# Kernel tuning notes

Hardware: AMD Instinct MI355X
Metric: run time of the kernel (lower is better)

## Reference

```python
import jax, jax.numpy as jnp
import numpy as np

# Multi-scale feature pyramid (H, W) per level
LEVEL_SHAPES = ((48, 160), (24, 80), (12, 40), (6, 20))
LEN = sum(h * w for h, w in LEVEL_SHAPES)  # 10200 flattened tokens
B, D, NH, NL, NP, DFF, NLAYERS = 2, 256, 8, 4, 4, 1024, 3
DH = D // NH
# offset normalizer is (W, H) per level, matching Deformable-DETR
NORMALIZER = np.array([[w, h] for h, w in LEVEL_SHAPES], dtype=np.float32)
LEVEL_START = np.cumsum([0] + [h * w for h, w in LEVEL_SHAPES])[:-1]


def layer_norm(x, g, b, eps=1e-5):
    m = jnp.mean(x, -1, keepdims=True)
    v = jnp.var(x, -1, keepdims=True)
    return (x - m) * jax.lax.rsqrt(v + eps) * g + b


def get_reference_points(valid_ratios):
    # valid_ratios: [B, NL, 2] (ratio_w, ratio_h)
    refs = []
    for lvl, (Hl, Wl) in enumerate(LEVEL_SHAPES):
        ry, rx = jnp.meshgrid(jnp.linspace(0.5, Hl - 0.5, Hl, dtype=jnp.float32),
                              jnp.linspace(0.5, Wl - 0.5, Wl, dtype=jnp.float32), indexing='ij')
        ry = ry.reshape(-1)[None] / (valid_ratios[:, None, lvl, 1] * Hl)
        rx = rx.reshape(-1)[None] / (valid_ratios[:, None, lvl, 0] * Wl)
        refs.append(jnp.stack([rx, ry], -1))
    ref = jnp.concatenate(refs, 1)                      # [B, LEN, 2]
    return ref[:, :, None] * valid_ratios[:, None]      # [B, LEN, NL, 2]


def bilinear_sample(value_bh, loc, Hl, Wl):
    # value_bh: [B, NH, Hl*Wl, DH]; loc: [B, Lq, NH, NP, 2] in [0,1]
    # grid_sample semantics: bilinear, zero padding, align_corners=False
    x = loc[..., 0] * Wl - 0.5
    y = loc[..., 1] * Hl - 0.5
    x0f = jnp.floor(x); y0f = jnp.floor(y)
    fx = x - x0f; fy = y - y0f
    x0 = x0f.astype(jnp.int32); y0 = y0f.astype(jnp.int32)
    Lq = loc.shape[1]
    out = jnp.zeros((B, NH, Lq * NP, DH), loc.dtype)
    for dy in (0, 1):
        for dx in (0, 1):
            xi = x0 + dx; yi = y0 + dy
            w = (fx if dx else 1.0 - fx) * (fy if dy else 1.0 - fy)
            valid = (xi >= 0) & (xi < Wl) & (yi >= 0) & (yi < Hl)
            idx = jnp.clip(yi, 0, Hl - 1) * Wl + jnp.clip(xi, 0, Wl - 1)  # [B,Lq,NH,NP]
            idx = jnp.transpose(idx, (0, 2, 1, 3)).reshape(B, NH, Lq * NP)
            v = jnp.take_along_axis(value_bh, idx[..., None], axis=2)    # [B,NH,Lq*NP,DH]
            wm = jnp.transpose(jnp.where(valid, w, 0.0), (0, 2, 1, 3)).reshape(B, NH, Lq * NP)
            out = out + v * wm[..., None]
    return out


def ms_deform_attn(q, src, ref, Woff, boff, Wattn, battn, Wval, bval, Wout, bout):
    Lq = q.shape[1]
    off = (q @ Woff + boff).reshape(B, Lq, NH, NL, NP, 2)
    attn = jax.nn.softmax((q @ Wattn + battn).reshape(B, Lq, NH, NL * NP), -1)
    attn = attn.reshape(B, Lq, NH, NL, NP)
    val = (src @ Wval + bval).reshape(B, LEN, NH, DH).transpose(0, 2, 1, 3)  # [B,NH,LEN,DH]
    norm = jnp.asarray(NORMALIZER)
    loc = ref[:, :, None, :, None, :] + off / norm[None, None, None, :, None, :]
    out = jnp.zeros((B, NH, Lq, DH), q.dtype)
    for lvl, (Hl, Wl) in enumerate(LEVEL_SHAPES):
        s = int(LEVEL_START[lvl])
        vl = val[:, :, s:s + Hl * Wl]
        sampled = bilinear_sample(vl, loc[:, :, :, lvl], Hl, Wl).reshape(B, NH, Lq, NP, DH)
        out = out + jnp.einsum('bhqpd,bqhp->bhqd', sampled, attn[:, :, :, lvl])
    out = out.transpose(0, 2, 1, 3).reshape(B, Lq, D)
    return out @ Wout + bout


def reference(src, pos, valid_ratios, W_off, b_off, W_attn, b_attn, W_val, b_val,
              W_out, b_out, ln1_g, ln1_b, W_ff1, b_ff1, W_ff2, b_ff2, ln2_g, ln2_b):
    ref = get_reference_points(valid_ratios)
    x = src
    for l in range(NLAYERS):
        q = x + pos
        att = ms_deform_attn(q, x, ref, W_off[l], b_off[l], W_attn[l], b_attn[l],
                             W_val[l], b_val[l], W_out[l], b_out[l])
        x = layer_norm(x + att, ln1_g[l], ln1_b[l])
        h = jax.nn.relu(x @ W_ff1[l] + b_ff1[l]) @ W_ff2[l] + b_ff2[l]
        x = layer_norm(x + h, ln2_g[l], ln2_b[l])
    return x


def setup_inputs() -> dict:
    key = jax.random.key(0)
    ks = jax.random.split(key, 12)
    s = 0.02
    return {
        'src': jax.random.normal(ks[0], (B, LEN, D), jnp.float32),
        'pos': jax.random.normal(ks[1], (B, LEN, D), jnp.float32),
        'valid_ratios': jnp.ones((B, NL, 2), jnp.float32),
        'W_off': jax.random.normal(ks[2], (NLAYERS, D, NH * NL * NP * 2), jnp.float32) * s,
        'b_off': jax.random.normal(ks[3], (NLAYERS, NH * NL * NP * 2), jnp.float32) * s,
        'W_attn': jax.random.normal(ks[4], (NLAYERS, D, NH * NL * NP), jnp.float32) * s,
        'b_attn': jax.random.normal(ks[5], (NLAYERS, NH * NL * NP), jnp.float32) * s,
        'W_val': jax.random.normal(ks[6], (NLAYERS, D, D), jnp.float32) * s,
        'b_val': jnp.zeros((NLAYERS, D), jnp.float32),
        'W_out': jax.random.normal(ks[7], (NLAYERS, D, D), jnp.float32) * s,
        'b_out': jnp.zeros((NLAYERS, D), jnp.float32),
        'ln1_g': jnp.ones((NLAYERS, D), jnp.float32),
        'ln1_b': jnp.zeros((NLAYERS, D), jnp.float32),
        'W_ff1': jax.random.normal(ks[8], (NLAYERS, D, DFF), jnp.float32) * s,
        'b_ff1': jnp.zeros((NLAYERS, DFF), jnp.float32),
        'W_ff2': jax.random.normal(ks[9], (NLAYERS, DFF, D), jnp.float32) * s,
        'b_ff2': jnp.zeros((NLAYERS, D), jnp.float32),
        'ln2_g': jnp.ones((NLAYERS, D), jnp.float32),
        'ln2_b': jnp.zeros((NLAYERS, D), jnp.float32),
    }
```

## Files before the change

kernel.cpp:

```cpp
#include <hip/hip_runtime.h>

typedef short bf16x8 __attribute__((ext_vector_type(8)));
typedef float f32x4  __attribute__((ext_vector_type(4)));

#define LEN_TOT 10200
#define BB 2
#define DD 256
#define NHH 8
#define NLL 4
#define NPP 4
#define DHH 32
#define DFF_ 1024
#define ROWS (BB * LEN_TOT)

__device__ inline unsigned short f2bf(float f) {
    unsigned int u = __float_as_uint(f);
    u += 0x7fffu + ((u >> 16) & 1u);
    return (unsigned short)(u >> 16);
}
__device__ inline unsigned int pack2(float a, float b) {
    return (unsigned int)f2bf(a) | ((unsigned int)f2bf(b) << 16);
}

__global__ __launch_bounds__(256) void ref_points_kernel(
    const float* __restrict__ vr, float* __restrict__ ref)
{
    int i = blockIdx.x * blockDim.x + threadIdx.x;
    if (i >= BB * LEN_TOT) return;
    int b = i / LEN_TOT, pos = i % LEN_TOT;
    int lvl, st, Hl, Wl;
    if (pos < 7680)      { lvl = 0; st = 0;     Hl = 48; Wl = 160; }
    else if (pos < 9600) { lvl = 1; st = 7680;  Hl = 24; Wl = 80;  }
    else if (pos < 10080){ lvl = 2; st = 9600;  Hl = 12; Wl = 40;  }
    else                 { lvl = 3; st = 10080; Hl = 6;  Wl = 20;  }
    int local = pos - st;
    int row = local / Wl, col = local % Wl;
    float rx = (col + 0.5f) / (vr[(b * NLL + lvl) * 2 + 0] * (float)Wl);
    float ry = (row + 0.5f) / (vr[(b * NLL + lvl) * 2 + 1] * (float)Hl);
    #pragma unroll
    for (int ol = 0; ol < NLL; ++ol) {
        ref[((size_t)i * NLL + ol) * 2 + 0] = rx * vr[(b * NLL + ol) * 2 + 0];
        ref[((size_t)i * NLL + ol) * 2 + 1] = ry * vr[(b * NLL + ol) * 2 + 1];
    }
}

__global__ __launch_bounds__(256) void convert_src_kernel(
    const float* __restrict__ src, float* __restrict__ x,
    unsigned short* __restrict__ xb, int n8)
{
    int i = blockIdx.x * blockDim.x + threadIdx.x;
    if (i >= n8) return;
    float4 a = ((const float4*)src)[2 * i];
    float4 b = ((const float4*)src)[2 * i + 1];
    ((float4*)x)[2 * i]     = a;
    ((float4*)x)[2 * i + 1] = b;
    uint4 o;
    o.x = pack2(a.x, a.y); o.y = pack2(a.z, a.w);
    o.z = pack2(b.x, b.y); o.w = pack2(b.z, b.w);
    ((uint4*)xb)[i] = o;
}

__global__ __launch_bounds__(256) void addq_kernel(
    const float* __restrict__ x, const float* __restrict__ p,
    unsigned short* __restrict__ qb, int n8)
{
    int i = blockIdx.x * blockDim.x + threadIdx.x;
    if (i >= n8) return;
    float4 a0 = ((const float4*)x)[2 * i];
    float4 a1 = ((const float4*)x)[2 * i + 1];
    float4 b0 = ((const float4*)p)[2 * i];
    float4 b1 = ((const float4*)p)[2 * i + 1];
    uint4 o;
    o.x = pack2(a0.x + b0.x, a0.y + b0.y);
    o.y = pack2(a0.z + b0.z, a0.w + b0.w);
    o.z = pack2(a1.x + b1.x, a1.y + b1.y);
    o.w = pack2(a1.z + b1.z, a1.w + b1.w);
    ((uint4*)qb)[i] = o;
}

__global__ __launch_bounds__(256) void wt_kernel(
    const float* __restrict__ W, unsigned short* __restrict__ WT,
    int K, int N, int ldOut, int rowOff)
{
    __shared__ float t[32][33];
    const float* Wl = W + (size_t)blockIdx.z * K * N;
    unsigned short* WTl = WT + (size_t)blockIdx.z * ldOut;
    int kb = blockIdx.x * 32, nb = blockIdx.y * 32;
    int tx = threadIdx.x, ty = threadIdx.y;
    #pragma unroll
    for (int i = 0; i < 4; ++i)
        t[ty + i * 8][tx] = Wl[(size_t)(kb + ty + i * 8) * N + nb + tx];
    __syncthreads();
    #pragma unroll
    for (int i = 0; i < 4; ++i)
        WTl[(size_t)(rowOff + nb + ty + i * 8) * K + kb + tx] = f2bf(t[tx][ty + i * 8]);
}

__global__ __launch_bounds__(256) void bias_oa_kernel(
    const float* __restrict__ b_off, const float* __restrict__ b_attn,
    float* __restrict__ out)
{
    int i = blockIdx.x * blockDim.x + threadIdx.x;
    if (i >= 3 * 384) return;
    int l = i / 384, j = i % 384;
    out[i] = (j < 256) ? b_off[l * 256 + j] : b_attn[l * 128 + (j - 256)];
}

template<int OUTMODE>
__global__ __launch_bounds__(256) void gemm_bf16(
    const unsigned short* __restrict__ A,
    const unsigned short* __restrict__ BT,
    const float* __restrict__ bias,
    void* __restrict__ Cout,
    int M, int N, int K)
{
    __shared__ short lds[2 * 128 * 64];
    const int tid = threadIdx.x;
    const int l   = tid & 63;
    const int wid = tid >> 6;
    const int wm  = wid >> 1, wn = wid & 1;
    const int lrow = l & 15, lkg = l >> 4;
    const int rowBase = blockIdx.x * 128;
    const int colBase = blockIdx.y * 128;

    const int srow  = tid >> 3;
    const int sslot = tid & 7;

    f32x4 acc[4][4] = {};

    for (int k0 = 0; k0 < K; k0 += 64) {
        #pragma unroll
        for (int rr = 0; rr < 128; rr += 32) {
            int r = rr + srow;
            int sw = (sslot ^ (r & 7)) * 8;
            int gr = rowBase + r; if (gr > M - 1) gr = M - 1;
            uint4 av = *(const uint4*)(A + (size_t)gr * K + k0 + sslot * 8);
            *(uint4*)&lds[r * 64 + sw] = av;
            int n = colBase + r;
            uint4 bv = *(const uint4*)(BT + (size_t)n * K + k0 + sslot * 8);
            *(uint4*)&lds[8192 + r * 64 + sw] = bv;
        }
        __syncthreads();
        #pragma unroll
        for (int kk = 0; kk < 2; ++kk) {
            int kslot = kk * 4 + lkg;
            int ssw = (kslot ^ (lrow & 7)) * 8;
            bf16x8 af[4], bfr[4];
            #pragma unroll
            for (int mi = 0; mi < 4; ++mi)
                af[mi] = *(const bf16x8*)&lds[(wm * 64 + mi * 16 + lrow) * 64 + ssw];
            #pragma unroll
            for (int ni = 0; ni < 4; ++ni)
                bfr[ni] = *(const bf16x8*)&lds[8192 + (wn * 64 + ni * 16 + lrow) * 64 + ssw];
            #pragma unroll
            for (int mi = 0; mi < 4; ++mi)
                #pragma unroll
                for (int ni = 0; ni < 4; ++ni)
                    acc[mi][ni] = __builtin_amdgcn_mfma_f32_16x16x32_bf16(
                        af[mi], bfr[ni], acc[mi][ni], 0, 0, 0);
        }
        __syncthreads();
    }

    #pragma unroll
    for (int ni = 0; ni < 4; ++ni) {
        int col = colBase + wn * 64 + ni * 16 + lrow;
        float bv = bias[col];
        #pragma unroll
        for (int mi = 0; mi < 4; ++mi) {
            int r0 = rowBase + wm * 64 + mi * 16 + lkg * 4;
            #pragma unroll
            for (int j = 0; j < 4; ++j) {
                int r = r0 + j;
                if (r < M) {
                    float v = acc[mi][ni][j] + bv;
                    if (OUTMODE == 0) {
                        ((float*)Cout)[(size_t)r * N + col] = v;
                    } else {
                        if (OUTMODE == 1) v = fmaxf(v, 0.f);
                        ((unsigned short*)Cout)[(size_t)r * N + col] = f2bf(v);
                    }
                }
            }
        }
    }
}

__global__ __launch_bounds__(256) void sample_kernel(
    const unsigned short* __restrict__ valb,
    const float* __restrict__ oa,
    const float* __restrict__ ref,
    unsigned short* __restrict__ out)
{
    __shared__ int2 ent[8][64];

    const int tid = threadIdx.x;
    const int il = tid >> 5;
    const int L  = tid & 31;
    const int item = blockIdx.x * 8 + il;
    const int h  = item & (NHH - 1);
    const int bq = item >> 3;
    const int b  = bq / LEN_TOT;

    const float* row = oa + (size_t)bq * 384;

    {
        int p = L >> 1, dy = L & 1;
        int lvl = p >> 2;
        int Wl = 160 >> lvl, Hl = 48 >> lvl;
        int ST = (lvl == 0) ? 0 : ((lvl == 1) ? 7680 : ((lvl == 2) ? 9600 : 10080));

        float logit = row[256 + h * 16 + p];
        float m = logit;
        #pragma unroll
        for (int mk = 1; mk <= 16; mk <<= 1) m = fmaxf(m, __shfl_xor(m, mk));
        float e = __expf(logit - m);
        float s = e;
        #pragma unroll
        for (int mk = 1; mk <= 16; mk <<= 1) s += __shfl_xor(s, mk);
        float a = 2.f * e / s;

        float rx = ref[bq * 8 + lvl * 2 + 0];
        float ry = ref[bq * 8 + lvl * 2 + 1];
        float ox = row[h * 32 + p * 2 + 0];
        float oy = row[h * 32 + p * 2 + 1];
        float xx = fmaf(rx, (float)Wl, ox) - 0.5f;
        float yy = fmaf(ry, (float)Hl, oy) - 0.5f;
        float xf = floorf(xx), yf = floorf(yy);
        float fx = xx - xf, fy = yy - yf;
        int x0 = (int)xf, y0 = (int)yf;
        int yi = y0 + dy;
        float wy = dy ? fy : 1.f - fy;
        bool vy = (yi >= 0) && (yi < Hl);
        int yc = min(max(yi, 0), Hl - 1);
        int base = (b * LEN_TOT + ST) * 256 + h * 32;
        #pragma unroll
        for (int dx = 0; dx < 2; ++dx) {
            int xi = x0 + dx;
            float wx = dx ? fx : 1.f - fx;
            bool valid = vy && (xi >= 0) && (xi < Wl);
            int xc = min(max(xi, 0), Wl - 1);
            float w = valid ? a * wx * wy : 0.f;
            ent[il][p * 4 + dy * 2 + dx] =
                make_int2(base + (yc * Wl + xc) * 256, __float_as_int(w));
        }
    }
    __syncthreads();

    float acc = 0.f;
    #pragma unroll 16
    for (int e2 = 0; e2 < 64; ++e2) {
        int2 d = ent[il][e2];
        unsigned short uv = valb[(size_t)d.x + L];
        float v = __uint_as_float((unsigned int)uv << 16);
        acc = fmaf(__int_as_float(d.y), v, acc);
    }
    out[(size_t)item * DHH + L] = f2bf(acc);
}

__global__ __launch_bounds__(256) void resln_kernel(
    float* __restrict__ x, const float* __restrict__ r,
    const float* __restrict__ g, const float* __restrict__ bta,
    unsigned short* __restrict__ xb)
{
    int row = blockIdx.x * 4 + (threadIdx.x >> 6);
    int lane = threadIdx.x & 63;
    if (row >= ROWS) return;
    float4 v  = *(const float4*)(x + (size_t)row * DD + lane * 4);
    float4 rr = *(const float4*)(r + (size_t)row * DD + lane * 4);
    v.x += rr.x; v.y += rr.y; v.z += rr.z; v.w += rr.w;
    float s  = v.x + v.y + v.z + v.w;
    float s2 = v.x * v.x + v.y * v.y + v.z * v.z + v.w * v.w;
    #pragma unroll
    for (int o = 1; o < 64; o <<= 1) {
        s  += __shfl_xor(s, o);
        s2 += __shfl_xor(s2, o);
    }
    float mean = s * (1.f / DD);
    float var  = s2 * (1.f / DD) - mean * mean;
    float inv  = rsqrtf(var + 1e-5f);
    float4 gg = *(const float4*)(g + lane * 4);
    float4 bb = *(const float4*)(bta + lane * 4);
    float4 o;
    o.x = (v.x - mean) * inv * gg.x + bb.x;
    o.y = (v.y - mean) * inv * gg.y + bb.y;
    o.z = (v.z - mean) * inv * gg.z + bb.z;
    o.w = (v.w - mean) * inv * gg.w + bb.w;
    *(float4*)(x + (size_t)row * DD + lane * 4) = o;
    uint2 ob;
    ob.x = pack2(o.x, o.y);
    ob.y = pack2(o.z, o.w);
    ((uint2*)(xb + (size_t)row * DD))[lane] = ob;
}

extern "C" void kernel_launch(void* const* d_in, const int* in_sizes, int n_in,
                              void* d_out, int out_size, void* d_ws, size_t ws_size,
                              hipStream_t stream)
{
    const float* src    = (const float*)d_in[0];
    const float* pos    = (const float*)d_in[1];
    const float* vr     = (const float*)d_in[2];
    const float* W_off  = (const float*)d_in[3];
    const float* b_off  = (const float*)d_in[4];
    const float* W_attn = (const float*)d_in[5];
    const float* b_attn = (const float*)d_in[6];
    const float* W_val  = (const float*)d_in[7];
    const float* b_val  = (const float*)d_in[8];
    const float* W_out  = (const float*)d_in[9];
    const float* b_out  = (const float*)d_in[10];
    const float* ln1_g  = (const float*)d_in[11];
    const float* ln1_b  = (const float*)d_in[12];
    const float* W_ff1  = (const float*)d_in[13];
    const float* b_ff1  = (const float*)d_in[14];
    const float* W_ff2  = (const float*)d_in[15];
    const float* b_ff2  = (const float*)d_in[16];
    const float* ln2_g  = (const float*)d_in[17];
    const float* ln2_b  = (const float*)d_in[18];

    float* x = (float*)d_out;
    float* ws = (float*)d_ws;
    size_t o = 0;
    float* oa      = ws + o; o += (size_t)ROWS * 384;
    float* tmp     = ws + o; o += (size_t)ROWS * 256;
    float* ref     = ws + o; o += (size_t)ROWS * 8;
    float* bias_oa = ws + o; o += 3 * 384;

    unsigned short* ub = (unsigned short*)(ws + o);
    size_t uo = 0;
    unsigned short* q_bf    = ub + uo; uo += (size_t)ROWS * 256;
    unsigned short* x_bf    = ub + uo; uo += (size_t)ROWS * 256;
    unsigned short* samp_bf = ub + uo; uo += (size_t)ROWS * 256;
    unsigned short* val_bf  = ub + uo; uo += (size_t)ROWS * 256;
    unsigned short* h_bf    = ub + uo; uo += (size_t)ROWS * DFF_;
    unsigned short* WT_oa   = ub + uo; uo += (size_t)3 * 384 * 256;
    unsigned short* WT_val  = ub + uo; uo += (size_t)3 * 256 * 256;
    unsigned short* WT_out  = ub + uo; uo += (size_t)3 * 256 * 256;
    unsigned short* WT_ff1  = ub + uo; uo += (size_t)3 * 256 * 1024;
    unsigned short* WT_ff2  = ub + uo; uo += (size_t)3 * 1024 * 256;

    const int n8 = ROWS * DD / 8;

    convert_src_kernel<<<(n8 + 255) / 256, 256, 0, stream>>>(src, x, x_bf, n8);
    ref_points_kernel<<<(ROWS + 255) / 256, 256, 0, stream>>>(vr, ref);

    dim3 wtb(32, 8);
    wt_kernel<<<dim3(8,  8, 3), wtb, 0, stream>>>(W_off,  WT_oa,  256, 256,  384 * 256, 0);
    wt_kernel<<<dim3(8,  4, 3), wtb, 0, stream>>>(W_attn, WT_oa,  256, 128,  384 * 256, 256);
    wt_kernel<<<dim3(8,  8, 3), wtb, 0, stream>>>(W_val,  WT_val, 256, 256,  256 * 256, 0);
    wt_kernel<<<dim3(8,  8, 3), wtb, 0, stream>>>(W_out,  WT_out, 256, 256,  256 * 256, 0);
    wt_kernel<<<dim3(8, 32, 3), wtb, 0, stream>>>(W_ff1,  WT_ff1, 256, 1024, 256 * 1024, 0);
    wt_kernel<<<dim3(32, 8, 3), wtb, 0, stream>>>(W_ff2,  WT_ff2, 1024, 256, 1024 * 256, 0);
    bias_oa_kernel<<<(3 * 384 + 255) / 256, 256, 0, stream>>>(b_off, b_attn, bias_oa);

    dim3 g384(160, 3), g256(160, 2), g1024(160, 8);

    for (int l = 0; l < 3; ++l) {
        addq_kernel<<<(n8 + 255) / 256, 256, 0, stream>>>(x, pos, q_bf, n8);
        gemm_bf16<0><<<g384, 256, 0, stream>>>(
            q_bf, WT_oa + (size_t)l * 384 * 256, bias_oa + (size_t)l * 384, oa,
            ROWS, 384, 256);
        gemm_bf16<2><<<g256, 256, 0, stream>>>(
            x_bf, WT_val + (size_t)l * 65536, b_val + (size_t)l * 256, val_bf,
            ROWS, 256, 256);
        sample_kernel<<<ROWS * NHH / 8, 256, 0, stream>>>(
            val_bf, oa, ref, samp_bf);
        gemm_bf16<0><<<g256, 256, 0, stream>>>(
            samp_bf, WT_out + (size_t)l * 65536, b_out + (size_t)l * 256, tmp,
            ROWS, 256, 256);
        resln_kernel<<<(ROWS + 3) / 4, 256, 0, stream>>>(
            x, tmp, ln1_g + (size_t)l * 256, ln1_b + (size_t)l * 256, x_bf);
        gemm_bf16<1><<<g1024, 256, 0, stream>>>(
            x_bf, WT_ff1 + (size_t)l * 262144, b_ff1 + (size_t)l * 1024, h_bf,
            ROWS, 1024, 256);
        gemm_bf16<0><<<g256, 256, 0, stream>>>(
            h_bf, WT_ff2 + (size_t)l * 262144, b_ff2 + (size_t)l * 256, tmp,
            ROWS, 256, 1024);
        resln_kernel<<<(ROWS + 3) / 4, 256, 0, stream>>>(
            x, tmp, ln2_g + (size_t)l * 256, ln2_b + (size_t)l * 256, x_bf);
    }
}
```

Baseline: 730.8 us.

## Fuse query add into LN, bf16 offsets, direct-to-LDS GEMM loads, vectorized sampling

The per-layer addq kernel is removed: the first q is built in the conversion kernel and later ones in the second residual-LayerNorm kernel. The offset/attention GEMM now writes bf16 instead of fp32, which halves that buffer's traffic but makes sampling offsets and logits less precise. GEMM tile loads use global_load_lds so data goes straight into LDS without passing through registers. The sampling gather now reads 8 bf16 values per lane with 16-byte loads and reduces across lanes with shuffles, replacing scalar 2-byte gathers.

```diff
diff --git a/kernel.cpp b/kernel.cpp
--- a/kernel.cpp
+++ b/kernel.cpp
@@ -21,6 +21,9 @@
 __device__ inline unsigned int pack2(float a, float b) {
     return (unsigned int)f2bf(a) | ((unsigned int)f2bf(b) << 16);
 }
+__device__ inline float bflo(unsigned int u) { return __uint_as_float(u << 16); }
+__device__ inline float bfhi(unsigned int u) { return __uint_as_float(u & 0xffff0000u); }
+__device__ inline float bfs(unsigned short u) { return __uint_as_float((unsigned int)u << 16); }
 
 __global__ __launch_bounds__(256) void ref_points_kernel(
     const float* __restrict__ vr, float* __restrict__ ref)
@@ -45,8 +48,9 @@
 }
 
 __global__ __launch_bounds__(256) void convert_src_kernel(
-    const float* __restrict__ src, float* __restrict__ x,
-    unsigned short* __restrict__ xb, int n8)
+    const float* __restrict__ src, const float* __restrict__ pos,
+    float* __restrict__ x, unsigned short* __restrict__ xb,
+    unsigned short* __restrict__ qb, int n8)
 {
     int i = blockIdx.x * blockDim.x + threadIdx.x;
     if (i >= n8) return;
@@ -58,24 +62,14 @@
     o.x = pack2(a.x, a.y); o.y = pack2(a.z, a.w);
     o.z = pack2(b.x, b.y); o.w = pack2(b.z, b.w);
     ((uint4*)xb)[i] = o;
-}
-
-__global__ __launch_bounds__(256) void addq_kernel(
-    const float* __restrict__ x, const float* __restrict__ p,
-    unsigned short* __restrict__ qb, int n8)
-{
-    int i = blockIdx.x * blockDim.x + threadIdx.x;
-    if (i >= n8) return;
-    float4 a0 = ((const float4*)x)[2 * i];
-    float4 a1 = ((const float4*)x)[2 * i + 1];
-    float4 b0 = ((const float4*)p)[2 * i];
-    float4 b1 = ((const float4*)p)[2 * i + 1];
-    uint4 o;
-    o.x = pack2(a0.x + b0.x, a0.y + b0.y);
-    o.y = pack2(a0.z + b0.z, a0.w + b0.w);
-    o.z = pack2(a1.x + b1.x, a1.y + b1.y);
-    o.w = pack2(a1.z + b1.z, a1.w + b1.w);
-    ((uint4*)qb)[i] = o;
+    float4 p0 = ((const float4*)pos)[2 * i];
+    float4 p1 = ((const float4*)pos)[2 * i + 1];
+    uint4 oq;
+    oq.x = pack2(a.x + p0.x, a.y + p0.y);
+    oq.y = pack2(a.z + p0.z, a.w + p0.w);
+    oq.z = pack2(b.x + p1.x, b.y + p1.y);
+    oq.w = pack2(b.z + p1.z, b.w + p1.w);
+    ((uint4*)qb)[i] = oq;
 }
 
 __global__ __launch_bounds__(256) void wt_kernel(
@@ -123,22 +117,25 @@
     const int rowBase = blockIdx.x * 128;
     const int colBase = blockIdx.y * 128;
 
-    const int srow  = tid >> 3;
-    const int sslot = tid & 7;
-
     f32x4 acc[4][4] = {};
 
     for (int k0 = 0; k0 < K; k0 += 64) {
         #pragma unroll
-        for (int rr = 0; rr < 128; rr += 32) {
-            int r = rr + srow;
-            int sw = (sslot ^ (r & 7)) * 8;
+        for (int it = 0; it < 4; ++it) {
+            int sidx = tid + 256 * it;
+            int r = sidx >> 3;
+            int ss = ((sidx & 7) ^ (r & 7)) * 8;
             int gr = rowBase + r; if (gr > M - 1) gr = M - 1;
-            uint4 av = *(const uint4*)(A + (size_t)gr * K + k0 + sslot * 8);
-            *(uint4*)&lds[r * 64 + sw] = av;
-            int n = colBase + r;
-            uint4 bv = *(const uint4*)(BT + (size_t)n * K + k0 + sslot * 8);
-            *(uint4*)&lds[8192 + r * 64 + sw] = bv;
+            __builtin_amdgcn_global_load_lds(
+                (const __attribute__((address_space(1))) unsigned int*)
+                    (A + (size_t)gr * K + k0 + ss),
+                (__attribute__((address_space(3))) unsigned int*)&lds[sidx * 8],
+                16, 0, 0);
+            __builtin_amdgcn_global_load_lds(
+                (const __attribute__((address_space(1))) unsigned int*)
+                    (BT + (size_t)(colBase + r) * K + k0 + ss),
+                (__attribute__((address_space(3))) unsigned int*)&lds[8192 + sidx * 8],
+                16, 0, 0);
         }
         __syncthreads();
         #pragma unroll
@@ -188,7 +185,7 @@
 
 __global__ __launch_bounds__(256) void sample_kernel(
     const unsigned short* __restrict__ valb,
-    const float* __restrict__ oa,
+    const unsigned short* __restrict__ oa,
     const float* __restrict__ ref,
     unsigned short* __restrict__ out)
 {
@@ -202,7 +199,7 @@
     const int bq = item >> 3;
     const int b  = bq / LEN_TOT;
 
-    const float* row = oa + (size_t)bq * 384;
+    const unsigned short* row = oa + (size_t)bq * 384;
 
     {
         int p = L >> 1, dy = L & 1;
@@ -210,7 +207,7 @@
         int Wl = 160 >> lvl, Hl = 48 >> lvl;
         int ST = (lvl == 0) ? 0 : ((lvl == 1) ? 7680 : ((lvl == 2) ? 9600 : 10080));
 
-        float logit = row[256 + h * 16 + p];
+        float logit = bfs(row[256 + h * 16 + p]);
         float m = logit;
         #pragma unroll
         for (int mk = 1; mk <= 16; mk <<= 1) m = fmaxf(m, __shfl_xor(m, mk));
@@ -222,8 +219,8 @@
 
         float rx = ref[bq * 8 + lvl * 2 + 0];
         float ry = ref[bq * 8 + lvl * 2 + 1];
-        float ox = row[h * 32 + p * 2 + 0];
-        float oy = row[h * 32 + p * 2 + 1];
+        float ox = bfs(row[h * 32 + p * 2 + 0]);
+        float oy = bfs(row[h * 32 + p * 2 + 1]);
         float xx = fmaf(rx, (float)Wl, ox) - 0.5f;
         float yy = fmaf(ry, (float)Hl, oy) - 0.5f;
         float xf = floorf(xx), yf = floorf(yy);
@@ -247,21 +244,40 @@
     }
     __syncthreads();
 
-    float acc = 0.f;
-    #pragma unroll 16
-    for (int e2 = 0; e2 < 64; ++e2) {
-        int2 d = ent[il][e2];
-        unsigned short uv = valb[(size_t)d.x + L];
-        float v = __uint_as_float((unsigned int)uv << 16);
-        acc = fmaf(__int_as_float(d.y), v, acc);
-    }
-    out[(size_t)item * DHH + L] = f2bf(acc);
+    const int oct = L & 3;
+    const int sub = L >> 2;
+    float a0 = 0.f, a1 = 0.f, a2 = 0.f, a3 = 0.f;
+    float a4 = 0.f, a5 = 0.f, a6 = 0.f, a7 = 0.f;
+    #pragma unroll
+    for (int i = 0; i < 8; ++i) {
+        int2 d = ent[il][sub + 8 * i];
+        float w = __int_as_float(d.y);
+        uint4 v = *(const uint4*)(valb + (size_t)(unsigned)d.x + oct * 8);
+        a0 = fmaf(w, bflo(v.x), a0); a1 = fmaf(w, bfhi(v.x), a1);
+        a2 = fmaf(w, bflo(v.y), a2); a3 = fmaf(w, bfhi(v.y), a3);
+        a4 = fmaf(w, bflo(v.z), a4); a5 = fmaf(w, bfhi(v.z), a5);
+        a6 = fmaf(w, bflo(v.w), a6); a7 = fmaf(w, bfhi(v.w), a7);
+    }
+    #pragma unroll
+    for (int mk = 4; mk <= 16; mk <<= 1) {
+        a0 += __shfl_xor(a0, mk); a1 += __shfl_xor(a1, mk);
+        a2 += __shfl_xor(a2, mk); a3 += __shfl_xor(a3, mk);
+        a4 += __shfl_xor(a4, mk); a5 += __shfl_xor(a5, mk);
+        a6 += __shfl_xor(a6, mk); a7 += __shfl_xor(a7, mk);
+    }
+    if (sub == 0) {
+        uint4 o;
+        o.x = pack2(a0, a1); o.y = pack2(a2, a3);
+        o.z = pack2(a4, a5); o.w = pack2(a6, a7);
+        *(uint4*)(out + (size_t)item * DHH + oct * 8) = o;
+    }
 }
 
 __global__ __launch_bounds__(256) void resln_kernel(
     float* __restrict__ x, const float* __restrict__ r,
     const float* __restrict__ g, const float* __restrict__ bta,
-    unsigned short* __restrict__ xb)
+    unsigned short* __restrict__ xb,
+    const float* __restrict__ pos, unsigned short* __restrict__ qb)
 {
     int row = blockIdx.x * 4 + (threadIdx.x >> 6);
     int lane = threadIdx.x & 63;
@@ -291,6 +307,13 @@
     ob.x = pack2(o.x, o.y);
     ob.y = pack2(o.z, o.w);
     ((uint2*)(xb + (size_t)row * DD))[lane] = ob;
+    if (qb) {
+        float4 pv = *(const float4*)(pos + (size_t)row * DD + lane * 4);
+        uint2 oq;
+        oq.x = pack2(o.x + pv.x, o.y + pv.y);
+        oq.y = pack2(o.z + pv.z, o.w + pv.w);
+        ((uint2*)(qb + (size_t)row * DD))[lane] = oq;
+    }
 }
 
 extern "C" void kernel_launch(void* const* d_in, const int* in_sizes, int n_in,
@@ -320,13 +343,13 @@
     float* x = (float*)d_out;
     float* ws = (float*)d_ws;
     size_t o = 0;
-    float* oa      = ws + o; o += (size_t)ROWS * 384;
     float* tmp     = ws + o; o += (size_t)ROWS * 256;
     float* ref     = ws + o; o += (size_t)ROWS * 8;
     float* bias_oa = ws + o; o += 3 * 384;
 
     unsigned short* ub = (unsigned short*)(ws + o);
     size_t uo = 0;
+    unsigned short* oa      = ub + uo; uo += (size_t)ROWS * 384;
     unsigned short* q_bf    = ub + uo; uo += (size_t)ROWS * 256;
     unsigned short* x_bf    = ub + uo; uo += (size_t)ROWS * 256;
     unsigned short* samp_bf = ub + uo; uo += (size_t)ROWS * 256;
@@ -340,7 +363,7 @@
 
     const int n8 = ROWS * DD / 8;
 
-    convert_src_kernel<<<(n8 + 255) / 256, 256, 0, stream>>>(src, x, x_bf, n8);
+    convert_src_kernel<<<(n8 + 255) / 256, 256, 0, stream>>>(src, pos, x, x_bf, q_bf, n8);
     ref_points_kernel<<<(ROWS + 255) / 256, 256, 0, stream>>>(vr, ref);
 
     dim3 wtb(32, 8);
@@ -355,8 +378,7 @@
     dim3 g384(160, 3), g256(160, 2), g1024(160, 8);
 
     for (int l = 0; l < 3; ++l) {
-        addq_kernel<<<(n8 + 255) / 256, 256, 0, stream>>>(x, pos, q_bf, n8);
-        gemm_bf16<0><<<g384, 256, 0, stream>>>(
+        gemm_bf16<2><<<g384, 256, 0, stream>>>(
             q_bf, WT_oa + (size_t)l * 384 * 256, bias_oa + (size_t)l * 384, oa,
             ROWS, 384, 256);
         gemm_bf16<2><<<g256, 256, 0, stream>>>(
@@ -368,7 +390,8 @@
             samp_bf, WT_out + (size_t)l * 65536, b_out + (size_t)l * 256, tmp,
             ROWS, 256, 256);
         resln_kernel<<<(ROWS + 3) / 4, 256, 0, stream>>>(
-            x, tmp, ln1_g + (size_t)l * 256, ln1_b + (size_t)l * 256, x_bf);
+            x, tmp, ln1_g + (size_t)l * 256, ln1_b + (size_t)l * 256, x_bf,
+            nullptr, nullptr);
         gemm_bf16<1><<<g1024, 256, 0, stream>>>(
             x_bf, WT_ff1 + (size_t)l * 262144, b_ff1 + (size_t)l * 1024, h_bf,
             ROWS, 1024, 256);
@@ -376,6 +399,7 @@
             h_bf, WT_ff2 + (size_t)l * 262144, b_ff2 + (size_t)l * 256, tmp,
             ROWS, 256, 1024);
         resln_kernel<<<(ROWS + 3) / 4, 256, 0, stream>>>(
-            x, tmp, ln2_g + (size_t)l * 256, ln2_b + (size_t)l * 256, x_bf);
-    }
-}
+            x, tmp, ln2_g + (size_t)l * 256, ln2_b + (size_t)l * 256, x_bf,
+            (l < 2) ? pos : nullptr, (l < 2) ? q_bf : nullptr);
+    }
+}
```

Result: faster. 694.7 us (-4.9%).
